# Performance work log

Hardware: AMD Instinct MI355X
Metric: run time of the kernel (lower is better)

The kernel has to match this reference:

```python
import jax, jax.numpy as jnp
import numpy as np

N_NODES = 50000
N_EDGES = 800000
D_IN = 96
D_OUT = 96
N_GRAPHS = 50


def setup_inputs() -> dict:
    key = jax.random.key(0)
    ks = jax.random.split(key, 16)
    s = 1.0 / np.sqrt(D_IN)
    inp = {
        "x": jax.random.normal(ks[0], (N_NODES, D_IN), jnp.float32),
        "edge_index": jax.random.randint(ks[1], (2, N_EDGES), 0, N_NODES, jnp.int32),
        "edge_attr": jax.random.uniform(ks[2], (N_EDGES, 1), jnp.float32),
        "batch": jnp.sort(jax.random.randint(ks[3], (N_NODES,), 0, N_GRAPHS, jnp.int32)),
        "w1_w": jax.random.normal(ks[4], (D_IN, D_OUT), jnp.float32) * s,
        "w1_b": jax.random.normal(ks[5], (D_OUT,), jnp.float32) * 0.01,
        "w2_w": jax.random.normal(ks[6], (D_IN, D_OUT), jnp.float32) * s,
        "w2_b": jax.random.normal(ks[7], (D_OUT,), jnp.float32) * 0.01,
        "w3_w": jax.random.normal(ks[8], (D_IN, D_OUT), jnp.float32) * s,
        "w3_b": jax.random.normal(ks[9], (D_OUT,), jnp.float32) * 0.01,
        "w4_w": jax.random.normal(ks[10], (D_IN, D_OUT), jnp.float32) * s,
        "w4_b": jax.random.normal(ks[11], (D_OUT,), jnp.float32) * 0.01,
        "w5_w": jax.random.normal(ks[12], (1, D_OUT), jnp.float32),
        "w5_b": jax.random.normal(ks[13], (D_OUT,), jnp.float32) * 0.01,
    }
    return inp


def reference(x, edge_index, edge_attr, batch,
              w1_w, w1_b, w2_w, w2_b, w3_w, w3_b, w4_w, w4_b, w5_w, w5_b):
    n = x.shape[0]
    src, dst = edge_index[0], edge_index[1]  # x_j = x[src], x_i = x[dst]
    sqrt_d = jnp.sqrt(jnp.asarray(D_OUT, x.dtype))

    x_i = x[dst]                                  # [E, D]
    x_j = x[src]                                  # [E, D]
    xi_t = x_i @ w3_w + w3_b                      # w3(x_i)
    xj_t = x_j @ w4_w + w4_b                      # w4(x_j)
    ea_t = edge_attr @ w5_w + w5_b                # w5(edge_attr), [E, D]

    scores = jnp.sum(xi_t * (xj_t + ea_t), axis=-1) / sqrt_d  # [E]

    # segment softmax over destination-node neighborhoods (PyG softmax)
    seg_max = jax.ops.segment_max(scores, dst, num_segments=n)
    ex = jnp.exp(scores - seg_max[dst])
    denom = jax.ops.segment_sum(ex, dst, num_segments=n)
    alpha = ex / (denom[dst] + jnp.asarray(1e-16, x.dtype))

    msg = alpha[:, None] * (x_j @ w2_w + w2_b)    # [E, D]
    aggr = jax.ops.segment_sum(msg, dst, num_segments=n)

    node_out = x @ w1_w + w1_b + aggr             # update: w1(x) + aggr

    # global mean pool per graph
    sums = jax.ops.segment_sum(node_out, batch, num_segments=N_GRAPHS)
    counts = jax.ops.segment_sum(jnp.ones((n,), x.dtype), batch, num_segments=N_GRAPHS)
    return sums / jnp.maximum(counts, 1.0)[:, None]
```

## Files before the change

### kernel.cpp

```cpp
#include <hip/hip_runtime.h>
#include <math.h>

#define D 96
#define RSQ 0.10206207261596577f
#define TSTRIDE 104

typedef __attribute__((ext_vector_type(8))) short short8;
typedef __attribute__((ext_vector_type(4))) float f32x4;

__device__ __forceinline__ unsigned short f2bf(float f){
  unsigned u = __float_as_uint(f);
  unsigned r = (u + 0x7fff + ((u >> 16) & 1)) >> 16;
  return (unsigned short)r;
}
__device__ __forceinline__ float bf2f(unsigned short h){
  return __uint_as_float(((unsigned)h) << 16);
}
__device__ __forceinline__ float bflo(unsigned u){ return __uint_as_float(u << 16); }
__device__ __forceinline__ float bfhi(unsigned u){ return __uint_as_float(u & 0xffff0000u); }
__device__ __forceinline__ int lbound(const int* __restrict__ a, int n, int v){
  int lo = 0, hi = n;
  while (lo < hi){ int mid = (lo + hi) >> 1; if (a[mid] < v) lo = mid + 1; else hi = mid; }
  return lo;
}

__global__ __launch_bounds__(256) void k_wprep_deg(
    const float* __restrict__ w1, const float* __restrict__ w2,
    const float* __restrict__ w3, const float* __restrict__ w4,
    unsigned short* __restrict__ wt_h, unsigned short* __restrict__ wt_l,
    const int* __restrict__ dstI, int* __restrict__ deg,
    int* __restrict__ rank, int E){
  int gtid = blockIdx.x * 256 + threadIdx.x;
  if (gtid < 4 * D * D){
    int m = gtid / (D * D);
    int r = gtid % (D * D);
    int nn = r / D, k = r % D;
    const float* w = (m == 0) ? w1 : (m == 1) ? w2 : (m == 2) ? w3 : w4;
    float v = w[k * D + nn];
    unsigned short h = f2bf(v);
    wt_h[gtid] = h;
    wt_l[gtid] = f2bf(v - bf2f(h));
  }
  if (gtid < E) rank[gtid] = atomicAdd(&deg[dstI[gtid]], 1);
}

__global__ __launch_bounds__(256) void k_transform_mfma(
    const float* __restrict__ x,
    const unsigned short* __restrict__ wt_h, const unsigned short* __restrict__ wt_l,
    const float* __restrict__ b1, const float* __restrict__ b2,
    const float* __restrict__ b3, const float* __restrict__ b4,
    const float* __restrict__ w5, const float* __restrict__ b5,
    float* __restrict__ acc_o, unsigned short* __restrict__ x24,
    float* __restrict__ x3o,
    float* __restrict__ p5, float* __restrict__ pb, int n){
  __shared__ __align__(16) unsigned short xs_h[32][TSTRIDE];
  __shared__ __align__(16) unsigned short xs_l[32][TSTRIDE];
  int tid = threadIdx.x;
  int n0 = blockIdx.x * 32;
  for (int e = tid; e < 32 * D; e += 256){
    int r = e / D, c = e % D;
    int node = n0 + r;
    float v = (node < n) ? x[(size_t)node * D + c] : 0.0f;
    unsigned short h = f2bf(v);
    xs_h[r][c] = h;
    xs_l[r][c] = f2bf(v - bf2f(h));
  }
  __syncthreads();

  int wv = tid >> 6;
  int lane = tid & 63;
  int lr = lane & 15;
  int kg = lane >> 4;

  f32x4 c00 = {0,0,0,0}, c01 = {0,0,0,0}, c02 = {0,0,0,0};
  f32x4 c03 = {0,0,0,0}, c04 = {0,0,0,0}, c05 = {0,0,0,0};
  f32x4 c10 = {0,0,0,0}, c11 = {0,0,0,0}, c12 = {0,0,0,0};
  f32x4 c13 = {0,0,0,0}, c14 = {0,0,0,0}, c15 = {0,0,0,0};
  const unsigned short* wtm_h = wt_h + (size_t)wv * D * D;
  const unsigned short* wtm_l = wt_l + (size_t)wv * D * D;

  #pragma unroll
  for (int k0 = 0; k0 < D; k0 += 32){
    int kb = k0 + kg * 8;
    short8 ah0 = *(const short8*)&xs_h[lr][kb];
    short8 al0 = *(const short8*)&xs_l[lr][kb];
    short8 ah1 = *(const short8*)&xs_h[lr + 16][kb];
    short8 al1 = *(const short8*)&xs_l[lr + 16][kb];
    #define NC_BODY(nc, C0, C1) { \
      int col = (nc) * 16 + lr; \
      short8 bh = *(const short8*)(wtm_h + col * D + kb); \
      short8 bl = *(const short8*)(wtm_l + col * D + kb); \
      C0 = __builtin_amdgcn_mfma_f32_16x16x32_bf16(ah0, bh, C0, 0, 0, 0); \
      C0 = __builtin_amdgcn_mfma_f32_16x16x32_bf16(ah0, bl, C0, 0, 0, 0); \
      C0 = __builtin_amdgcn_mfma_f32_16x16x32_bf16(al0, bh, C0, 0, 0, 0); \
      C1 = __builtin_amdgcn_mfma_f32_16x16x32_bf16(ah1, bh, C1, 0, 0, 0); \
      C1 = __builtin_amdgcn_mfma_f32_16x16x32_bf16(ah1, bl, C1, 0, 0, 0); \
      C1 = __builtin_amdgcn_mfma_f32_16x16x32_bf16(al1, bh, C1, 0, 0, 0); }
    NC_BODY(0, c00, c10) NC_BODY(1, c01, c11) NC_BODY(2, c02, c12)
    NC_BODY(3, c03, c13) NC_BODY(4, c04, c14) NC_BODY(5, c05, c15)
    #undef NC_BODY
  }

  const float* bias = (wv == 0) ? b1 : (wv == 1) ? b2 : (wv == 2) ? b3 : b4;
  f32x4 p5a0 = {0,0,0,0}, p5a1 = {0,0,0,0};
  f32x4 pba0 = {0,0,0,0}, pba1 = {0,0,0,0};

  #define EPI_BODY(nc, C0, C1) { \
    int col = (nc) * 16 + lr; \
    float bb = bias[col]; \
    float w5v = w5[col], b5v = b5[col]; \
    _Pragma("unroll") \
    for (int q = 0; q < 4; ++q){ \
      float v0e = C0[q] + bb; \
      float v1e = C1[q] + bb; \
      int row0 = kg * 4 + q, row1 = 16 + kg * 4 + q; \
      if (n0 + row0 < n){ \
        if (wv == 0) acc_o[(size_t)(n0 + row0) * D + col] = v0e; \
        else if (wv == 1) x24[(size_t)(n0 + row0) * 192 + 96 + col] = f2bf(v0e); \
        else if (wv == 2) x3o[(size_t)(n0 + row0) * D + col] = v0e; \
        else x24[(size_t)(n0 + row0) * 192 + col] = f2bf(v0e); \
      } \
      if (n0 + row1 < n){ \
        if (wv == 0) acc_o[(size_t)(n0 + row1) * D + col] = v1e; \
        else if (wv == 1) x24[(size_t)(n0 + row1) * 192 + 96 + col] = f2bf(v1e); \
        else if (wv == 2) x3o[(size_t)(n0 + row1) * D + col] = v1e; \
        else x24[(size_t)(n0 + row1) * 192 + col] = f2bf(v1e); \
      } \
      p5a0[q] += v0e * w5v; pba0[q] += v0e * b5v; \
      p5a1[q] += v1e * w5v; pba1[q] += v1e * b5v; \
    } }
  EPI_BODY(0, c00, c10) EPI_BODY(1, c01, c11) EPI_BODY(2, c02, c12)
  EPI_BODY(3, c03, c13) EPI_BODY(4, c04, c14) EPI_BODY(5, c05, c15)
  #undef EPI_BODY

  if (wv == 2){
    #pragma unroll
    for (int off = 1; off < 16; off <<= 1){
      #pragma unroll
      for (int q = 0; q < 4; ++q){
        p5a0[q] += __shfl_xor(p5a0[q], off); pba0[q] += __shfl_xor(pba0[q], off);
        p5a1[q] += __shfl_xor(p5a1[q], off); pba1[q] += __shfl_xor(pba1[q], off);
      }
    }
    if (lr == 0){
      #pragma unroll
      for (int q = 0; q < 4; ++q){
        int row0 = kg * 4 + q, row1 = 16 + kg * 4 + q;
        if (n0 + row0 < n){ p5[n0 + row0] = p5a0[q]; pb[n0 + row0] = pba0[q]; }
        if (n0 + row1 < n){ p5[n0 + row1] = p5a1[q]; pb[n0 + row1] = pba1[q]; }
      }
    }
  }
}

__global__ __launch_bounds__(256) void k_scanA(
    const int* __restrict__ deg, int* __restrict__ rowp,
    int* __restrict__ partials, int n){
  __shared__ int ws[4];
  int tid = threadIdx.x, lane = tid & 63, wid = tid >> 6;
  int i = blockIdx.x * 256 + tid;
  int v = (i < n) ? deg[i] : 0;
  int s = v;
  #pragma unroll
  for (int off = 1; off < 64; off <<= 1){ int u = __shfl_up(s, off); if (lane >= off) s += u; }
  if (lane == 63) ws[wid] = s;
  __syncthreads();
  if (tid < 4){
    int u = ws[tid];
    #pragma unroll
    for (int off = 1; off < 4; off <<= 1){ int q = __shfl_up(u, off); if (tid >= off) u += q; }
    ws[tid] = u;
  }
  __syncthreads();
  int woff = wid ? ws[wid - 1] : 0;
  if (i < n) rowp[i] = woff + s - v;
  if (tid == 255) partials[blockIdx.x] = ws[3];
}

__global__ __launch_bounds__(256) void k_scanB(
    int* __restrict__ partials, int* __restrict__ rowp, int nb, int n){
  __shared__ int ws[4];
  int tid = threadIdx.x, lane = tid & 63, wid = tid >> 6;
  int running = 0;
  for (int base = 0; base < nb; base += 256){
    int i = base + tid;
    int v = (i < nb) ? partials[i] : 0;
    int s = v;
    #pragma unroll
    for (int off = 1; off < 64; off <<= 1){ int u = __shfl_up(s, off); if (lane >= off) s += u; }
    if (lane == 63) ws[wid] = s;
    __syncthreads();
    if (tid < 4){
      int u = ws[tid];
      #pragma unroll
      for (int off = 1; off < 4; off <<= 1){ int q = __shfl_up(u, off); if (tid >= off) u += q; }
      ws[tid] = u;
    }
    __syncthreads();
    int woff = wid ? ws[wid - 1] : 0;
    if (i < nb) partials[i] = running + woff + s - v;
    running += ws[3];
    __syncthreads();
  }
  if (tid == 0) rowp[n] = running;
}

__global__ __launch_bounds__(256) void k_scatter(
    const int* __restrict__ srcI, const int* __restrict__ dstI,
    const float* __restrict__ eattr, const int* __restrict__ rowp,
    const int* __restrict__ partials, const int* __restrict__ rank,
    int2* __restrict__ sortedSE, int E){
  int e = blockIdx.x * blockDim.x + threadIdx.x;
  if (e >= E) return;
  int t = dstI[e];
  int pos = rowp[t] + partials[t >> 8] + rank[e];
  sortedSE[pos] = make_int2(srcI[e], __float_as_int(eattr[e]));
}

__global__ __launch_bounds__(256) void k_attn(
    const unsigned short* __restrict__ x24, const float* __restrict__ x3,
    const float* __restrict__ p5,
    const float* __restrict__ pb, const int2* __restrict__ sortedSE,
    const int* __restrict__ rowp, const int* __restrict__ partials,
    float* __restrict__ node_acc, int n){
  int t = blockIdx.x * 4 + (threadIdx.x >> 6);
  int lane = threadIdx.x & 63;
  if (t >= n) return;
  int beg = rowp[t] + partials[t >> 8];
  int end = (t + 1 < n) ? (rowp[t + 1] + partials[(t + 1) >> 8]) : rowp[n];
  if (beg == end) return;
  int j = lane & 15;
  int g = lane >> 4;

  const float2* r3 = (const float2*)(x3 + (size_t)t * D);
  float2 v0 = r3[j], v1 = r3[j + 16], v2 = r3[j + 32];
  float p5t = p5[t], pbt = pb[t];

  float m = -INFINITY, dsum = 0.0f;
  float a0 = 0, a1 = 0, a2 = 0, a3 = 0, a4 = 0, a5 = 0;

  for (int c = beg; c < end; c += 8){
    int eA = c + g, eB = c + 4 + g;
    bool actA = eA < end, actB = eB < end;
    int2 seA = sortedSE[actA ? eA : end - 1];
    int2 seB = sortedSE[actB ? eB : end - 1];
    const unsigned* rA = (const unsigned*)(x24 + (size_t)seA.x * 192);
    const unsigned* rB = (const unsigned*)(x24 + (size_t)seB.x * 192);
    unsigned uA0 = rA[j], uA1 = rA[j + 16], uA2 = rA[j + 32];
    unsigned uB0 = rB[j], uB1 = rB[j + 16], uB2 = rB[j + 32];
    float sA = v0.x * bflo(uA0) + v0.y * bfhi(uA0)
             + v1.x * bflo(uA1) + v1.y * bfhi(uA1)
             + v2.x * bflo(uA2) + v2.y * bfhi(uA2);
    float sB = v0.x * bflo(uB0) + v0.y * bfhi(uB0)
             + v1.x * bflo(uB1) + v1.y * bfhi(uB1)
             + v2.x * bflo(uB2) + v2.y * bfhi(uB2);
    sA += __shfl_xor(sA, 1); sA += __shfl_xor(sA, 2);
    sA += __shfl_xor(sA, 4); sA += __shfl_xor(sA, 8);
    sB += __shfl_xor(sB, 1); sB += __shfl_xor(sB, 2);
    sB += __shfl_xor(sB, 4); sB += __shfl_xor(sB, 8);
    float scA = actA ? (sA + __int_as_float(seA.y) * p5t + pbt) * RSQ : -INFINITY;
    float scB = actB ? (sB + __int_as_float(seB.y) * p5t + pbt) * RSQ : -INFINITY;
    float mc = fmaxf(scA, scB);
    mc = fmaxf(mc, __shfl_xor(mc, 16));
    mc = fmaxf(mc, __shfl_xor(mc, 32));
    if (mc > m){
      float r = __expf(m - mc);
      dsum *= r; a0 *= r; a1 *= r; a2 *= r; a3 *= r; a4 *= r; a5 *= r;
      m = mc;
    }
    float wA = __expf(scA - m);
    float wB = __expf(scB - m);
    dsum += wA + wB;
    unsigned qA0 = rA[48 + j], qA1 = rA[48 + j + 16], qA2 = rA[48 + j + 32];
    unsigned qB0 = rB[48 + j], qB1 = rB[48 + j + 16], qB2 = rB[48 + j + 32];
    a0 += wA * bflo(qA0) + wB * bflo(qB0);
    a1 += wA * bfhi(qA0) + wB * bfhi(qB0);
    a2 += wA * bflo(qA1) + wB * bflo(qB1);
    a3 += wA * bfhi(qA1) + wB * bfhi(qB1);
    a4 += wA * bflo(qA2) + wB * bflo(qB2);
    a5 += wA * bfhi(qA2) + wB * bfhi(qB2);
  }
  a0 += __shfl_xor(a0, 16); a0 += __shfl_xor(a0, 32);
  a1 += __shfl_xor(a1, 16); a1 += __shfl_xor(a1, 32);
  a2 += __shfl_xor(a2, 16); a2 += __shfl_xor(a2, 32);
  a3 += __shfl_xor(a3, 16); a3 += __shfl_xor(a3, 32);
  a4 += __shfl_xor(a4, 16); a4 += __shfl_xor(a4, 32);
  a5 += __shfl_xor(a5, 16); a5 += __shfl_xor(a5, 32);
  dsum += __shfl_xor(dsum, 16); dsum += __shfl_xor(dsum, 32);
  float inv = 1.0f / (dsum + 1e-16f);
  if (lane < 16){
    size_t o = (size_t)t * D + 2 * j;
    node_acc[o]      += a0 * inv;
    node_acc[o + 1]  += a1 * inv;
    node_acc[o + 32] += a2 * inv;
    node_acc[o + 33] += a3 * inv;
    node_acc[o + 64] += a4 * inv;
    node_acc[o + 65] += a5 * inv;
  }
}

__global__ __launch_bounds__(96) void k_pool(
    const float* __restrict__ node_out, const int* __restrict__ batch,
    float* __restrict__ sums, int n){
  int g = blockIdx.x;
  int chunk = blockIdx.y, nch = gridDim.y;
  int lo = lbound(batch, n, g);
  int hi = lbound(batch, n, g + 1);
  int cnt = hi - lo;
  if (cnt <= 0) return;
  int per = (cnt + nch - 1) / nch;
  int b = lo + chunk * per;
  int e = min(b + per, hi);
  if (b >= e) return;
  int d = threadIdx.x;
  float s = 0.0f;
  for (int r = b; r < e; ++r) s += node_out[(size_t)r * D + d];
  atomicAdd(&sums[g * D + d], s);
}

__global__ __launch_bounds__(256) void k_final(
    const float* __restrict__ sums, const int* __restrict__ batch,
    float* __restrict__ out, int n, int total){
  int i = blockIdx.x * blockDim.x + threadIdx.x;
  if (i >= total) return;
  int g = i / D;
  int lo = lbound(batch, n, g);
  int hi = lbound(batch, n, g + 1);
  float c = (float)((hi - lo) > 1 ? (hi - lo) : 1);
  out[i] = sums[i] / c;
}

extern "C" void kernel_launch(void* const* d_in, const int* in_sizes, int n_in,
                              void* d_out, int out_size, void* d_ws, size_t ws_size,
                              hipStream_t stream){
  const float* x     = (const float*)d_in[0];
  const int*   eidx  = (const int*)d_in[1];
  const float* eattr = (const float*)d_in[2];
  const int*   batch = (const int*)d_in[3];
  const float* w1 = (const float*)d_in[4];
  const float* b1 = (const float*)d_in[5];
  const float* w2 = (const float*)d_in[6];
  const float* b2 = (const float*)d_in[7];
  const float* w3 = (const float*)d_in[8];
  const float* b3 = (const float*)d_in[9];
  const float* w4 = (const float*)d_in[10];
  const float* b4 = (const float*)d_in[11];
  const float* w5 = (const float*)d_in[12];
  const float* b5 = (const float*)d_in[13];
  float* out = (float*)d_out;

  const int N = in_sizes[0] / D;
  const int E = in_sizes[2];
  const int* srcI = eidx;
  const int* dstI = eidx + E;
  const int NB = (N + 255) / 256;
  const int NT = (N + 31) / 32;

  char* base = (char*)d_ws;
  size_t off = 0;
  auto alloc = [&](size_t bytes) -> char* {
    char* p = base + off;
    off = (off + bytes + 255) & ~(size_t)255;
    return p;
  };
  char* zbase = base;
  int*   deg   = (int*)alloc((size_t)N * 4);
  float* sums  = (float*)alloc((size_t)out_size * 4);
  size_t zbytes = off;
  float* node_acc = (float*)alloc((size_t)N * D * 4);
  unsigned short* x24 = (unsigned short*)alloc((size_t)N * 192 * 2);
  float* x3v      = (float*)alloc((size_t)N * D * 4);
  float* p5       = (float*)alloc((size_t)N * 4);
  float* pb       = (float*)alloc((size_t)N * 4);
  int*   rowp     = (int*)alloc((size_t)(N + 1) * 4);
  int*   partials = (int*)alloc((size_t)(NB + 1) * 4);
  int*   rank     = (int*)alloc((size_t)E * 4);
  int2*  sortedSE = (int2*)alloc((size_t)E * 8);
  unsigned short* wt_h = (unsigned short*)alloc((size_t)4 * D * D * 2);
  unsigned short* wt_l = (unsigned short*)alloc((size_t)4 * D * D * 2);
  (void)ws_size; (void)n_in;

  hipMemsetAsync(zbase, 0, zbytes, stream);

  k_wprep_deg<<<dim3((E + 255) / 256), dim3(256), 0, stream>>>(
      w1, w2, w3, w4, wt_h, wt_l, dstI, deg, rank, E);
  k_transform_mfma<<<dim3(NT), dim3(256), 0, stream>>>(
      x, wt_h, wt_l, b1, b2, b3, b4, w5, b5,
      node_acc, x24, x3v, p5, pb, N);
  k_scanA<<<dim3(NB), dim3(256), 0, stream>>>(deg, rowp, partials, N);
  k_scanB<<<dim3(1), dim3(256), 0, stream>>>(partials, rowp, NB, N);
  k_scatter<<<dim3((E + 255) / 256), dim3(256), 0, stream>>>(
      srcI, dstI, eattr, rowp, partials, rank, sortedSE, E);
  k_attn<<<dim3((N + 3) / 4), dim3(256), 0, stream>>>(
      x24, x3v, p5, pb, sortedSE, rowp, partials, node_acc, N);
  k_pool<<<dim3(out_size / D, 32), dim3(D), 0, stream>>>(node_acc, batch, sums, N);
  k_final<<<dim3((out_size + 255) / 256), dim3(256), 0, stream>>>(
      sums, batch, out, N, out_size);
}
```

Baseline: 273.2 us.

## Stage split weights in LDS with persistent grid-stride transform blocks

The transform kernel now runs as a persistent grid of at most 256 blocks. Each block loads all four hi/lo bf16 weight matrices into LDS once, about 147KB, then loops over 16-node tiles instead of one 32-node tile per block. This removes repeated global/L2 reads of the weights for every tile. In exchange, the large LDS footprint allows only one block per CU, each wave does half the MFMA work per tile, and the 256-block grid may underuse a GPU with 256 CUs and limit latency hiding on the x loads.

```diff
diff --git a/kernel.cpp b/kernel.cpp
--- a/kernel.cpp
+++ b/kernel.cpp
@@ -3,7 +3,6 @@
 
 #define D 96
 #define RSQ 0.10206207261596577f
-#define TSTRIDE 104
 
 typedef __attribute__((ext_vector_type(8))) short short8;
 typedef __attribute__((ext_vector_type(4))) float f32x4;
@@ -52,102 +51,96 @@
     const float* __restrict__ w5, const float* __restrict__ b5,
     float* __restrict__ acc_o, unsigned short* __restrict__ x24,
     float* __restrict__ x3o,
-    float* __restrict__ p5, float* __restrict__ pb, int n){
-  __shared__ __align__(16) unsigned short xs_h[32][TSTRIDE];
-  __shared__ __align__(16) unsigned short xs_l[32][TSTRIDE];
+    float* __restrict__ p5, float* __restrict__ pb, int n, int NT){
+  __shared__ __align__(16) unsigned short wlds[4][2][D * D];
+  __shared__ __align__(16) unsigned short xs_h[16][104];
+  __shared__ __align__(16) unsigned short xs_l[16][104];
   int tid = threadIdx.x;
-  int n0 = blockIdx.x * 32;
-  for (int e = tid; e < 32 * D; e += 256){
-    int r = e / D, c = e % D;
-    int node = n0 + r;
-    float v = (node < n) ? x[(size_t)node * D + c] : 0.0f;
-    unsigned short h = f2bf(v);
-    xs_h[r][c] = h;
-    xs_l[r][c] = f2bf(v - bf2f(h));
-  }
-  __syncthreads();
+
+  {
+    const short8* gh = (const short8*)wt_h;
+    const short8* gl = (const short8*)wt_l;
+    for (int c = tid; c < 4 * D * D / 8; c += 256){
+      int m = c / (D * D / 8);
+      int r = c - m * (D * D / 8);
+      *(short8*)&wlds[m][0][r * 8] = gh[c];
+      *(short8*)&wlds[m][1][r * 8] = gl[c];
+    }
+  }
 
   int wv = tid >> 6;
-  int lane = tid & 63;
-  int lr = lane & 15;
-  int kg = lane >> 4;
-
-  f32x4 c00 = {0,0,0,0}, c01 = {0,0,0,0}, c02 = {0,0,0,0};
-  f32x4 c03 = {0,0,0,0}, c04 = {0,0,0,0}, c05 = {0,0,0,0};
-  f32x4 c10 = {0,0,0,0}, c11 = {0,0,0,0}, c12 = {0,0,0,0};
-  f32x4 c13 = {0,0,0,0}, c14 = {0,0,0,0}, c15 = {0,0,0,0};
-  const unsigned short* wtm_h = wt_h + (size_t)wv * D * D;
-  const unsigned short* wtm_l = wt_l + (size_t)wv * D * D;
-
-  #pragma unroll
-  for (int k0 = 0; k0 < D; k0 += 32){
-    int kb = k0 + kg * 8;
-    short8 ah0 = *(const short8*)&xs_h[lr][kb];
-    short8 al0 = *(const short8*)&xs_l[lr][kb];
-    short8 ah1 = *(const short8*)&xs_h[lr + 16][kb];
-    short8 al1 = *(const short8*)&xs_l[lr + 16][kb];
-    #define NC_BODY(nc, C0, C1) { \
-      int col = (nc) * 16 + lr; \
-      short8 bh = *(const short8*)(wtm_h + col * D + kb); \
-      short8 bl = *(const short8*)(wtm_l + col * D + kb); \
-      C0 = __builtin_amdgcn_mfma_f32_16x16x32_bf16(ah0, bh, C0, 0, 0, 0); \
-      C0 = __builtin_amdgcn_mfma_f32_16x16x32_bf16(ah0, bl, C0, 0, 0, 0); \
-      C0 = __builtin_amdgcn_mfma_f32_16x16x32_bf16(al0, bh, C0, 0, 0, 0); \
-      C1 = __builtin_amdgcn_mfma_f32_16x16x32_bf16(ah1, bh, C1, 0, 0, 0); \
-      C1 = __builtin_amdgcn_mfma_f32_16x16x32_bf16(ah1, bl, C1, 0, 0, 0); \
-      C1 = __builtin_amdgcn_mfma_f32_16x16x32_bf16(al1, bh, C1, 0, 0, 0); }
-    NC_BODY(0, c00, c10) NC_BODY(1, c01, c11) NC_BODY(2, c02, c12)
-    NC_BODY(3, c03, c13) NC_BODY(4, c04, c14) NC_BODY(5, c05, c15)
-    #undef NC_BODY
-  }
-
+  int lane = tid & 63, lr = lane & 15, kg = lane >> 4;
+  const unsigned short* Wh = &wlds[wv][0][0];
+  const unsigned short* Wl = &wlds[wv][1][0];
   const float* bias = (wv == 0) ? b1 : (wv == 1) ? b2 : (wv == 2) ? b3 : b4;
-  f32x4 p5a0 = {0,0,0,0}, p5a1 = {0,0,0,0};
-  f32x4 pba0 = {0,0,0,0}, pba1 = {0,0,0,0};
-
-  #define EPI_BODY(nc, C0, C1) { \
-    int col = (nc) * 16 + lr; \
-    float bb = bias[col]; \
-    float w5v = w5[col], b5v = b5[col]; \
-    _Pragma("unroll") \
-    for (int q = 0; q < 4; ++q){ \
-      float v0e = C0[q] + bb; \
-      float v1e = C1[q] + bb; \
-      int row0 = kg * 4 + q, row1 = 16 + kg * 4 + q; \
-      if (n0 + row0 < n){ \
-        if (wv == 0) acc_o[(size_t)(n0 + row0) * D + col] = v0e; \
-        else if (wv == 1) x24[(size_t)(n0 + row0) * 192 + 96 + col] = f2bf(v0e); \
-        else if (wv == 2) x3o[(size_t)(n0 + row0) * D + col] = v0e; \
-        else x24[(size_t)(n0 + row0) * 192 + col] = f2bf(v0e); \
-      } \
-      if (n0 + row1 < n){ \
-        if (wv == 0) acc_o[(size_t)(n0 + row1) * D + col] = v1e; \
-        else if (wv == 1) x24[(size_t)(n0 + row1) * 192 + 96 + col] = f2bf(v1e); \
-        else if (wv == 2) x3o[(size_t)(n0 + row1) * D + col] = v1e; \
-        else x24[(size_t)(n0 + row1) * 192 + col] = f2bf(v1e); \
-      } \
-      p5a0[q] += v0e * w5v; pba0[q] += v0e * b5v; \
-      p5a1[q] += v1e * w5v; pba1[q] += v1e * b5v; \
-    } }
-  EPI_BODY(0, c00, c10) EPI_BODY(1, c01, c11) EPI_BODY(2, c02, c12)
-  EPI_BODY(3, c03, c13) EPI_BODY(4, c04, c14) EPI_BODY(5, c05, c15)
-  #undef EPI_BODY
-
-  if (wv == 2){
-    #pragma unroll
-    for (int off = 1; off < 16; off <<= 1){
+
+  for (int tile = blockIdx.x; tile < NT; tile += gridDim.x){
+    int n0 = tile * 16;
+    __syncthreads();
+    for (int e = tid; e < 16 * D; e += 256){
+      int r = e / D, cc = e % D;
+      int node = n0 + r;
+      float v = (node < n) ? x[(size_t)node * D + cc] : 0.0f;
+      unsigned short h = f2bf(v);
+      xs_h[r][cc] = h;
+      xs_l[r][cc] = f2bf(v - bf2f(h));
+    }
+    __syncthreads();
+
+    f32x4 acc[6];
+    #pragma unroll
+    for (int i = 0; i < 6; ++i) acc[i] = (f32x4){0, 0, 0, 0};
+    #pragma unroll
+    for (int k0i = 0; k0i < 3; ++k0i){
+      int kb = k0i * 32 + kg * 8;
+      short8 ah = *(const short8*)&xs_h[lr][kb];
+      short8 al = *(const short8*)&xs_l[lr][kb];
+      #pragma unroll
+      for (int nc = 0; nc < 6; ++nc){
+        int col = nc * 16 + lr;
+        short8 bh = *(const short8*)(Wh + col * D + kb);
+        short8 bl = *(const short8*)(Wl + col * D + kb);
+        acc[nc] = __builtin_amdgcn_mfma_f32_16x16x32_bf16(ah, bh, acc[nc], 0, 0, 0);
+        acc[nc] = __builtin_amdgcn_mfma_f32_16x16x32_bf16(ah, bl, acc[nc], 0, 0, 0);
+        acc[nc] = __builtin_amdgcn_mfma_f32_16x16x32_bf16(al, bh, acc[nc], 0, 0, 0);
+      }
+    }
+
+    f32x4 p5a = {0, 0, 0, 0}, pba = {0, 0, 0, 0};
+    #pragma unroll
+    for (int nc = 0; nc < 6; ++nc){
+      int col = nc * 16 + lr;
+      float bb = bias[col];
+      float w5v = w5[col], b5v = b5[col];
       #pragma unroll
       for (int q = 0; q < 4; ++q){
-        p5a0[q] += __shfl_xor(p5a0[q], off); pba0[q] += __shfl_xor(pba0[q], off);
-        p5a1[q] += __shfl_xor(p5a1[q], off); pba1[q] += __shfl_xor(pba1[q], off);
+        float v = acc[nc][q] + bb;
+        int row = kg * 4 + q;
+        if (n0 + row < n){
+          if (wv == 0) acc_o[(size_t)(n0 + row) * D + col] = v;
+          else if (wv == 1) x24[(size_t)(n0 + row) * 192 + 96 + col] = f2bf(v);
+          else if (wv == 2) x3o[(size_t)(n0 + row) * D + col] = v;
+          else x24[(size_t)(n0 + row) * 192 + col] = f2bf(v);
+        }
+        p5a[q] += v * w5v;
+        pba[q] += v * b5v;
       }
     }
-    if (lr == 0){
+    if (wv == 2){
       #pragma unroll
-      for (int q = 0; q < 4; ++q){
-        int row0 = kg * 4 + q, row1 = 16 + kg * 4 + q;
-        if (n0 + row0 < n){ p5[n0 + row0] = p5a0[q]; pb[n0 + row0] = pba0[q]; }
-        if (n0 + row1 < n){ p5[n0 + row1] = p5a1[q]; pb[n0 + row1] = pba1[q]; }
+      for (int off = 1; off < 16; off <<= 1){
+        #pragma unroll
+        for (int q = 0; q < 4; ++q){
+          p5a[q] += __shfl_xor(p5a[q], off);
+          pba[q] += __shfl_xor(pba[q], off);
+        }
+      }
+      if (lr == 0){
+        #pragma unroll
+        for (int q = 0; q < 4; ++q){
+          int row = kg * 4 + q;
+          if (n0 + row < n){ p5[n0 + row] = p5a[q]; pb[n0 + row] = pba[q]; }
+        }
       }
     }
   }
@@ -354,7 +347,8 @@
   const int* srcI = eidx;
   const int* dstI = eidx + E;
   const int NB = (N + 255) / 256;
-  const int NT = (N + 31) / 32;
+  const int NT = (N + 15) / 16;
+  const int TGRID = (NT < 256) ? NT : 256;
 
   char* base = (char*)d_ws;
   size_t off = 0;
@@ -384,9 +378,9 @@
 
   k_wprep_deg<<<dim3((E + 255) / 256), dim3(256), 0, stream>>>(
       w1, w2, w3, w4, wt_h, wt_l, dstI, deg, rank, E);
-  k_transform_mfma<<<dim3(NT), dim3(256), 0, stream>>>(
+  k_transform_mfma<<<dim3(TGRID), dim3(256), 0, stream>>>(
       x, wt_h, wt_l, b1, b2, b3, b4, w5, b5,
-      node_acc, x24, x3v, p5, pb, N);
+      node_acc, x24, x3v, p5, pb, N, NT);
   k_scanA<<<dim3(NB), dim3(256), 0, stream>>>(deg, rowp, partials, N);
   k_scanB<<<dim3(1), dim3(256), 0, stream>>>(partials, rowp, NB, N);
   k_scatter<<<dim3((E + 255) / 256), dim3(256), 0, stream>>>(
```

Measured after the change: 308.9 us. 13.1% more time.
